# Performance work log

Measured on AMD Instinct MI355X. Metric: run time of the kernel, lower is better.

The kernel has to match this reference:

```python
import jax, jax.numpy as jnp
import numpy as np

N = 50000
E = 800000
IN_DIM = 256
HID = 256
OUT_DIM = 2


def setup_inputs() -> dict:
    key = jax.random.key(0)
    ks = jax.random.split(key, 10)
    x = jax.random.normal(ks[0], (N, IN_DIM), dtype=jnp.float32)
    edge_index = jax.random.randint(ks[1], (2, E), 0, N, dtype=jnp.int64)
    # Glorot-ish scaling so activations stay well-conditioned through 4 layers
    def w(k, fan_in, fan_out):
        return jax.random.normal(k, (fan_in, fan_out), dtype=jnp.float32) / jnp.sqrt(jnp.float32(fan_in))
    return {
        "x": x,
        "edge_index": edge_index,
        "W0": w(ks[2], IN_DIM, HID), "b0": jnp.zeros((HID,), jnp.float32),
        "W1": w(ks[3], HID, HID),    "b1": jnp.zeros((HID,), jnp.float32),
        "W2": w(ks[4], HID, HID),    "b2": jnp.zeros((HID,), jnp.float32),
        "W3": w(ks[5], HID, OUT_DIM), "b3": jnp.zeros((OUT_DIM,), jnp.float32),
    }


def _gcn_norm(edge_index, n, dtype):
    # PyG gcn_norm with self-loops: deg over destination, norm = d^-1/2[src]*d^-1/2[dst]
    loops = jnp.arange(n, dtype=edge_index.dtype)
    src = jnp.concatenate([edge_index[0], loops])
    dst = jnp.concatenate([edge_index[1], loops])
    deg = jax.ops.segment_sum(jnp.ones_like(dst, dtype=dtype), dst, num_segments=n)
    dis = deg ** -0.5  # deg >= 1 due to self-loops
    norm = dis[src] * dis[dst]
    return src, dst, norm


def reference(x, edge_index, W0, b0, W1, b1, W2, b2, W3, b3):
    n = x.shape[0]
    src, dst, norm = _gcn_norm(edge_index, n, x.dtype)

    def conv(h, W, b):
        h = h @ W                              # [N, F_out] dense GEMM
        msg = h[src] * norm[:, None]           # edge-gather + scale
        agg = jax.ops.segment_sum(msg, dst, num_segments=n)  # scatter-add
        return agg + b

    h = jax.nn.relu(conv(x, W0, b0))
    h = jax.nn.relu(conv(h, W1, b1))
    h = jax.nn.relu(conv(h, W2, b2))
    return conv(h, W3, b3)
```

## Files before the change

### kernel.cpp

```cpp
#include <hip/hip_runtime.h>

#define N_NODES 50000
#define N_EDGES 800000

static inline int cdiv(int a, int b) { return (a + b - 1) / b; }

typedef __attribute__((ext_vector_type(8))) short bf16x8;
typedef __attribute__((ext_vector_type(4))) float f32x4;
typedef __attribute__((ext_vector_type(2))) float f32x2;
typedef __attribute__((ext_vector_type(4))) unsigned int u32x4;

static __device__ __forceinline__ unsigned short f2bf(float f) {
    unsigned int u = __float_as_uint(f);
    unsigned int r = (u + 0x7FFF + ((u >> 16) & 1)) >> 16;
    return (unsigned short)r;
}
static __device__ __forceinline__ float bf2f(unsigned short h) {
    return __uint_as_float((unsigned int)h << 16);
}
static __device__ __forceinline__ float bf_lo(unsigned int u) { return __uint_as_float(u << 16); }
static __device__ __forceinline__ float bf_hi(unsigned int u) { return __uint_as_float(u & 0xFFFF0000u); }

static __device__ __forceinline__ int logc(int p) {
    int pl = p & 63;
    return (p & ~63) + (pl & 3) * 16 + (pl >> 2);
}

static __device__ __forceinline__ int2 ldnt2(const int2* p) {
    unsigned long long u = __builtin_nontemporal_load((const unsigned long long*)p);
    int2 r;
    r.x = (int)(u & 0xFFFFFFFFull);
    r.y = (int)(u >> 32);
    return r;
}

static __device__ __forceinline__ void acc8p(f32x2* acc, uint4 v, float wgt) {
    f32x2 w2;
    w2.x = wgt;
    w2.y = wgt;
    f32x2 p;
    p.x = bf_lo(v.x); p.y = bf_hi(v.x); acc[0] += p * w2;
    p.x = bf_lo(v.y); p.y = bf_hi(v.y); acc[1] += p * w2;
    p.x = bf_lo(v.z); p.y = bf_hi(v.z); acc[2] += p * w2;
    p.x = bf_lo(v.w); p.y = bf_hi(v.w); acc[3] += p * w2;
}


__global__ void k_count(const int* __restrict__ edst, int* cnt, int e) {
    int i = (blockIdx.x * 256 + threadIdx.x) * 4;
    if (i + 3 < e) {
        int4 v = *(const int4*)(edst + i);
        atomicAdd(&cnt[v.x], 1);
        atomicAdd(&cnt[v.y], 1);
        atomicAdd(&cnt[v.z], 1);
        atomicAdd(&cnt[v.w], 1);
    } else {
        for (int k = i; k < e; ++k) atomicAdd(&cnt[edst[k]], 1);
    }
}

__global__ __launch_bounds__(256) void k_scan1(const int* __restrict__ cnt,
                                               int* __restrict__ row_ptr,
                                               float* __restrict__ dis,
                                               int* __restrict__ blk, int n) {
    __shared__ int sums[256];
    int t = threadIdx.x;
    int base = blockIdx.x * 1024 + t * 4;
    int c0 = 0, c1 = 0, c2 = 0, c3 = 0;
    if (base + 3 < n) {
        int4 v = *(const int4*)(cnt + base);
        c0 = v.x + 1; c1 = v.y + 1; c2 = v.z + 1; c3 = v.w + 1;
    } else {
        if (base + 0 < n) c0 = cnt[base + 0] + 1;
        if (base + 1 < n) c1 = cnt[base + 1] + 1;
        if (base + 2 < n) c2 = cnt[base + 2] + 1;
        if (base + 3 < n) c3 = cnt[base + 3] + 1;
    }
    int s = c0 + c1 + c2 + c3;
    sums[t] = s;
    __syncthreads();
    int x = s;
    for (int off = 1; off < 256; off <<= 1) {
        int y = (t >= off) ? sums[t - off] : 0;
        __syncthreads();
        x += y;
        sums[t] = x;
        __syncthreads();
    }
    int excl = x - s;
    if (base + 0 < n) { row_ptr[base + 0] = excl;                dis[base + 0] = rsqrtf((float)c0); }
    if (base + 1 < n) { row_ptr[base + 1] = excl + c0;           dis[base + 1] = rsqrtf((float)c1); }
    if (base + 2 < n) { row_ptr[base + 2] = excl + c0 + c1;      dis[base + 2] = rsqrtf((float)c2); }
    if (base + 3 < n) { row_ptr[base + 3] = excl + c0 + c1 + c2; dis[base + 3] = rsqrtf((float)c3); }
    if (t == 255) blk[blockIdx.x] = x;
}

__global__ __launch_bounds__(256) void k_scan2(int* __restrict__ blk,
                                               int* __restrict__ row_ptr_n, int nb) {
    __shared__ int sums[256];
    int t = threadIdx.x;
    int s = (t < nb) ? blk[t] : 0;
    sums[t] = s;
    __syncthreads();
    int x = s;
    for (int off = 1; off < 256; off <<= 1) {
        int y = (t >= off) ? sums[t - off] : 0;
        __syncthreads();
        x += y;
        sums[t] = x;
        __syncthreads();
    }
    if (t < nb) blk[t] = x - s;
    if (t == 255) row_ptr_n[0] = x;
}

__global__ __launch_bounds__(256) void k_scan3(int* __restrict__ row_ptr,
                                               int* __restrict__ pos,
                                               const int* __restrict__ blk, int n) {
    int base = blockIdx.x * 1024 + threadIdx.x * 4;
    int off = blk[blockIdx.x];
#pragma unroll
    for (int i = 0; i < 4; ++i) {
        int idx = base + i;
        if (idx < n) {
            int v = row_ptr[idx] + off;
            row_ptr[idx] = v;
            pos[idx] = v;
        }
    }
}

__global__ void k_fill(const int* __restrict__ esrc, const int* __restrict__ edst,
                       int* pos, const float* __restrict__ dis,
                       int2* __restrict__ eg, int e, int n) {
    int i = blockIdx.x * 256 + threadIdx.x;
    if (i < e) {
        int s = esrc[i], d = edst[i];
        int p = atomicAdd(&pos[d], 1);
        unsigned long long u = (unsigned long long)(unsigned int)s |
                               ((unsigned long long)(unsigned int)__float_as_int(dis[s] * dis[d]) << 32);
        __builtin_nontemporal_store(u, (unsigned long long*)&eg[p]);
    } else if (i < e + n) {
        int v = i - e;
        int p = atomicAdd(&pos[v], 1);
        float dv = dis[v];
        unsigned long long u = (unsigned long long)(unsigned int)v |
                               ((unsigned long long)(unsigned int)__float_as_int(dv * dv) << 32);
        __builtin_nontemporal_store(u, (unsigned long long*)&eg[p]);
    }
}


__global__ __launch_bounds__(256) void k_prep(const float* __restrict__ W0,
                                              const float* __restrict__ W1,
                                              const float* __restrict__ W2,
                                              const float* __restrict__ b0,
                                              const float* __restrict__ b1,
                                              const float* __restrict__ b2,
                                              const float* __restrict__ W3,
                                              unsigned short* __restrict__ Wth,
                                              unsigned short* __restrict__ Wtl,
                                              float* __restrict__ bpw,
                                              const float* __restrict__ X,
                                              unsigned short* __restrict__ Xh, long total4) {
    if (blockIdx.x < 768) {
        int layer = blockIdx.x >> 8;
        int n = blockIdx.x & 255;
        int p = threadIdx.x;
        const float* W = layer == 0 ? W0 : (layer == 1 ? W1 : W2);
        int k = (layer != 0) ? logc(p) : p;
        float v = W[(size_t)k * 256 + n];
        unsigned short h = f2bf(v);
        size_t o = (size_t)layer * 65536 + (size_t)n * 256 + p;
        Wth[o] = h;
        Wtl[o] = f2bf(v - bf2f(h));
    } else if (blockIdx.x == 768) {
        int p = threadIdx.x;
        int c = logc(p);
        bpw[p] = b0[c];
        bpw[256 + p] = b1[c];
        bpw[512 + p] = b2[c];
        bpw[768 + p * 2 + 0] = W3[(size_t)c * 2 + 0];
        bpw[768 + p * 2 + 1] = W3[(size_t)c * 2 + 1];
    } else {
        long i = (long)(blockIdx.x - 769) * 256 + threadIdx.x;
        if (i >= total4) return;
        float4 v = *(const float4*)(X + i * 4);
        ushort4 h;
        h.x = f2bf(v.x);
        h.y = f2bf(v.y);
        h.z = f2bf(v.z);
        h.w = f2bf(v.w);
        *(ushort4*)(Xh + i * 4) = h;
    }
}


#define GEMM_RB 196

__global__ __launch_bounds__(256, 4) void k_gemm_mfma(const unsigned short* __restrict__ Ah,
                                                      const unsigned short* __restrict__ Wth,
                                                      const unsigned short* __restrict__ Wtl,
                                                      unsigned short* __restrict__ C, int M) {
    __shared__ unsigned short Wh[64][264];
    int rowblk = blockIdx.x % GEMM_RB;
    int colblk = blockIdx.x / GEMM_RB;
    int c0 = colblk * 64;
    int m0 = rowblk * 256;
    int t = threadIdx.x;
    int sr = t >> 2;

    {
        int hk0 = (t & 3) * 64;
        const unsigned short* gh = Wth + (size_t)(c0 + sr) * 256 + hk0;
        unsigned short* lh = &Wh[sr][hk0];
#pragma unroll
        for (int i = 0; i < 8; ++i)
            *(uint4*)(lh + i * 8) = *(const uint4*)(gh + i * 8);
    }
    __syncthreads();

    int lane = t & 63, wave = t >> 6;
    int quad = lane >> 4, l16 = lane & 15;

    const unsigned short* aph[4];
#pragma unroll
    for (int mt = 0; mt < 4; ++mt) {
        int m = m0 + wave * 64 + mt * 16 + l16;
        if (m >= M) m = M - 1;
        aph[mt] = Ah + (size_t)m * 256 + quad * 8;
    }
    const unsigned short* blp = Wtl + (size_t)(c0 + l16) * 256 + quad * 8;

    f32x4 acc[4][4];
#pragma unroll
    for (int i = 0; i < 4; ++i)
#pragma unroll
        for (int j = 0; j < 4; ++j) acc[i][j] = (f32x4){0.f, 0.f, 0.f, 0.f};

#pragma unroll 2
    for (int kc = 0; kc < 8; ++kc) {
        int ko = kc * 32;
        bf16x8 ahf[4];
#pragma unroll
        for (int mt = 0; mt < 4; ++mt) ahf[mt] = *(const bf16x8*)(aph[mt] + ko);
#pragma unroll
        for (int nt = 0; nt < 4; ++nt) {
            bf16x8 bh = *(const bf16x8*)&Wh[nt * 16 + l16][ko + quad * 8];
            bf16x8 bl = *(const bf16x8*)(blp + nt * 16 * 256 + ko);
#pragma unroll
            for (int mt = 0; mt < 4; ++mt) {
                acc[mt][nt] = __builtin_amdgcn_mfma_f32_16x16x32_bf16(ahf[mt], bh, acc[mt][nt], 0, 0, 0);
                acc[mt][nt] = __builtin_amdgcn_mfma_f32_16x16x32_bf16(ahf[mt], bl, acc[mt][nt], 0, 0, 0);
            }
        }
    }

#pragma unroll
    for (int mt = 0; mt < 4; ++mt) {
#pragma unroll
        for (int r = 0; r < 4; ++r) {
            int row = m0 + wave * 64 + mt * 16 + quad * 4 + r;
            if (row < M) {
                ushort4 sv;
                sv.x = f2bf(acc[mt][0][r]);
                sv.y = f2bf(acc[mt][1][r]);
                sv.z = f2bf(acc[mt][2][r]);
                sv.w = f2bf(acc[mt][3][r]);
                *(ushort4*)(C + (size_t)row * 256 + c0 + l16 * 4) = sv;
            }
        }
    }
}


template <int MODE>
__global__ __launch_bounds__(256, 8) void k_agg256(const unsigned short* __restrict__ t,
                                                   const int* __restrict__ row_ptr,
                                                   const int2* __restrict__ eg,
                                                   const float* __restrict__ bp,
                                                   unsigned short* __restrict__ outh,
                                                   const float* __restrict__ w3p,
                                                   float* __restrict__ t2, int n) {
    int lane = threadIdx.x & 63;
    int wave = threadIdx.x >> 6;
    int half = lane >> 5;
    int fl = lane & 31;
    const unsigned short* tp = t + fl * 8;
    int stride = gridDim.x * 4;

    for (int node = blockIdx.x * 4 + wave; node < n; node += stride) {
        int beg = row_ptr[node], end = row_ptr[node + 1];
        f32x2 acc2[4];
#pragma unroll
        for (int i = 0; i < 4; ++i) { acc2[i].x = 0.f; acc2[i].y = 0.f; }

        int e = beg + half;
        for (; e + 10 < end; e += 12) {
            int2 a0 = ldnt2(eg + e), a1 = ldnt2(eg + e + 2), a2 = ldnt2(eg + e + 4);
            int2 a3 = ldnt2(eg + e + 6), a4 = ldnt2(eg + e + 8), a5 = ldnt2(eg + e + 10);
            uint4 v0 = *(const uint4*)(tp + (size_t)a0.x * 256);
            uint4 v1 = *(const uint4*)(tp + (size_t)a1.x * 256);
            uint4 v2 = *(const uint4*)(tp + (size_t)a2.x * 256);
            uint4 v3 = *(const uint4*)(tp + (size_t)a3.x * 256);
            uint4 v4 = *(const uint4*)(tp + (size_t)a4.x * 256);
            uint4 v5 = *(const uint4*)(tp + (size_t)a5.x * 256);
            acc8p(acc2, v0, __int_as_float(a0.y));
            acc8p(acc2, v1, __int_as_float(a1.y));
            acc8p(acc2, v2, __int_as_float(a2.y));
            acc8p(acc2, v3, __int_as_float(a3.y));
            acc8p(acc2, v4, __int_as_float(a4.y));
            acc8p(acc2, v5, __int_as_float(a5.y));
        }
        for (; e + 6 < end; e += 8) {
            int2 a0 = ldnt2(eg + e), a1 = ldnt2(eg + e + 2);
            int2 a2 = ldnt2(eg + e + 4), a3 = ldnt2(eg + e + 6);
            uint4 v0 = *(const uint4*)(tp + (size_t)a0.x * 256);
            uint4 v1 = *(const uint4*)(tp + (size_t)a1.x * 256);
            uint4 v2 = *(const uint4*)(tp + (size_t)a2.x * 256);
            uint4 v3 = *(const uint4*)(tp + (size_t)a3.x * 256);
            acc8p(acc2, v0, __int_as_float(a0.y));
            acc8p(acc2, v1, __int_as_float(a1.y));
            acc8p(acc2, v2, __int_as_float(a2.y));
            acc8p(acc2, v3, __int_as_float(a3.y));
        }
        for (; e + 2 < end; e += 4) {
            int2 a0 = ldnt2(eg + e), a1 = ldnt2(eg + e + 2);
            uint4 v0 = *(const uint4*)(tp + (size_t)a0.x * 256);
            uint4 v1 = *(const uint4*)(tp + (size_t)a1.x * 256);
            acc8p(acc2, v0, __int_as_float(a0.y));
            acc8p(acc2, v1, __int_as_float(a1.y));
        }
        if (e < end) {
            int2 a0 = ldnt2(eg + e);
            uint4 v0 = *(const uint4*)(tp + (size_t)a0.x * 256);
            acc8p(acc2, v0, __int_as_float(a0.y));
        }

        float va[8];
#pragma unroll
        for (int i = 0; i < 4; ++i) { va[2 * i] = acc2[i].x; va[2 * i + 1] = acc2[i].y; }
#pragma unroll
        for (int i = 0; i < 8; ++i) va[i] += __shfl_xor(va[i], 32);

        if (MODE == 0) {
            if (half == 0) {
                float4 bA = *(const float4*)(bp + fl * 8);
                float4 bB = *(const float4*)(bp + fl * 8 + 4);
                float r0 = fmaxf(va[0] + bA.x, 0.f), r1 = fmaxf(va[1] + bA.y, 0.f);
                float r2 = fmaxf(va[2] + bA.z, 0.f), r3 = fmaxf(va[3] + bA.w, 0.f);
                float r4 = fmaxf(va[4] + bB.x, 0.f), r5 = fmaxf(va[5] + bB.y, 0.f);
                float r6 = fmaxf(va[6] + bB.z, 0.f), r7 = fmaxf(va[7] + bB.w, 0.f);
                u32x4 w;
                w.x = (unsigned)f2bf(r0) | ((unsigned)f2bf(r1) << 16);
                w.y = (unsigned)f2bf(r2) | ((unsigned)f2bf(r3) << 16);
                w.z = (unsigned)f2bf(r4) | ((unsigned)f2bf(r5) << 16);
                w.w = (unsigned)f2bf(r6) | ((unsigned)f2bf(r7) << 16);
                __builtin_nontemporal_store(w, (u32x4*)(outh + (size_t)node * 256 + fl * 8));
            }
        } else {
            float4 bA = *(const float4*)(bp + fl * 8);
            float4 bB = *(const float4*)(bp + fl * 8 + 4);
            float r0 = fmaxf(va[0] + bA.x, 0.f), r1 = fmaxf(va[1] + bA.y, 0.f);
            float r2 = fmaxf(va[2] + bA.z, 0.f), r3 = fmaxf(va[3] + bA.w, 0.f);
            float r4 = fmaxf(va[4] + bB.x, 0.f), r5 = fmaxf(va[5] + bB.y, 0.f);
            float r6 = fmaxf(va[6] + bB.z, 0.f), r7 = fmaxf(va[7] + bB.w, 0.f);
            const float* wp = w3p + fl * 16;
            float4 wA = *(const float4*)(wp + 0);
            float4 wB = *(const float4*)(wp + 4);
            float4 wC = *(const float4*)(wp + 8);
            float4 wD = *(const float4*)(wp + 12);
            float s0 = r0 * wA.x + r1 * wA.z + r2 * wB.x + r3 * wB.z +
                       r4 * wC.x + r5 * wC.z + r6 * wD.x + r7 * wD.z;
            float s1 = r0 * wA.y + r1 * wA.w + r2 * wB.y + r3 * wB.w +
                       r4 * wC.y + r5 * wC.w + r6 * wD.y + r7 * wD.w;
#pragma unroll
            for (int off = 16; off > 0; off >>= 1) {
                s0 += __shfl_xor(s0, off);
                s1 += __shfl_xor(s1, off);
            }
            if (lane == 0) {
                f32x2 o;
                o.x = s0;
                o.y = s1;
                __builtin_nontemporal_store(o, (f32x2*)(t2 + (size_t)node * 2));
            }
        }
    }
}


__global__ void k_agg2(const float* __restrict__ t2,
                       const int* __restrict__ row_ptr,
                       const int2* __restrict__ eg,
                       const float* __restrict__ b3,
                       float* __restrict__ out, int n) {
    int tid = blockIdx.x * 256 + threadIdx.x;
    int node = tid >> 2;
    int sub = tid & 3;
    if (node >= n) return;
    int beg = row_ptr[node], end = row_ptr[node + 1];
    float a0 = 0.f, a1 = 0.f;
    for (int e = beg + sub; e < end; e += 4) {
        int2 m = ldnt2(eg + e);
        float w = __int_as_float(m.y);
        float2 v = *(const float2*)(t2 + (size_t)m.x * 2);
        a0 += w * v.x;
        a1 += w * v.y;
    }
    a0 += __shfl_xor(a0, 1); a1 += __shfl_xor(a1, 1);
    a0 += __shfl_xor(a0, 2); a1 += __shfl_xor(a1, 2);
    if (sub == 0) {
        out[(size_t)node * 2 + 0] = a0 + b3[0];
        out[(size_t)node * 2 + 1] = a1 + b3[1];
    }
}


extern "C" void kernel_launch(void* const* d_in, const int* in_sizes, int n_in,
                              void* d_out, int out_size, void* d_ws, size_t ws_size,
                              hipStream_t stream) {
    const int N = N_NODES, E = N_EDGES;
    const float* x  = (const float*)d_in[0];
    const int* ei   = (const int*)d_in[1];
    const int* esrc = ei;
    const int* edst = ei + E;
    const float* W0 = (const float*)d_in[2];
    const float* b0 = (const float*)d_in[3];
    const float* W1 = (const float*)d_in[4];
    const float* b1 = (const float*)d_in[5];
    const float* W2 = (const float*)d_in[6];
    const float* b2 = (const float*)d_in[7];
    const float* W3 = (const float*)d_in[8];
    const float* b3 = (const float*)d_in[9];
    float* out = (float*)d_out;

    unsigned short* Ahh = (unsigned short*)d_ws;
    unsigned short* Tb  = Ahh + (size_t)N * 256;
    unsigned short* Wth = Tb + (size_t)N * 256;
    unsigned short* Wtl = Wth + 3 * 65536;
    int2*  eg     = (int2*)(Wtl + 3 * 65536);
    float* t2     = (float*)(eg + (E + N));
    float* bpw    = t2 + (size_t)N * 2;
    float* dis    = bpw + 1280;
    int*   cnt    = (int*)(dis + N);
    int*   row_ptr= cnt + N;
    int*   pos    = row_ptr + (N + 1);
    int*   blk    = pos + N;

    const int NB = cdiv(N, 1024);

    hipMemsetAsync(cnt, 0, (size_t)N * sizeof(int), stream);
    k_count<<<cdiv(E, 1024), 256, 0, stream>>>(edst, cnt, E);
    k_scan1<<<NB, 256, 0, stream>>>(cnt, row_ptr, dis, blk, N);
    k_scan2<<<1, 256, 0, stream>>>(blk, row_ptr + N, NB);
    k_scan3<<<NB, 256, 0, stream>>>(row_ptr, pos, blk, N);
    k_fill<<<cdiv(E + N, 256), 256, 0, stream>>>(esrc, edst, pos, dis, eg, E, N);

    const int ggrid = GEMM_RB * 4;
    const int agrid = 2048;
    const long total4 = (long)N * 64;
    const int CA = cdiv((int)total4, 256);

    k_prep<<<769 + CA, 256, 0, stream>>>(W0, W1, W2, b0, b1, b2, W3, Wth, Wtl, bpw, x, Ahh, total4);

    k_gemm_mfma<<<ggrid, 256, 0, stream>>>(Ahh, Wth, Wtl, Tb, N);
    k_agg256<0><<<agrid, 256, 0, stream>>>(Tb, row_ptr, eg, bpw, Ahh, nullptr, nullptr, N);
    k_gemm_mfma<<<ggrid, 256, 0, stream>>>(Ahh, Wth + 65536, Wtl + 65536, Tb, N);
    k_agg256<0><<<agrid, 256, 0, stream>>>(Tb, row_ptr, eg, bpw + 256, Ahh, nullptr, nullptr, N);
    k_gemm_mfma<<<ggrid, 256, 0, stream>>>(Ahh, Wth + 2 * 65536, Wtl + 2 * 65536, Tb, N);
    k_agg256<1><<<agrid, 256, 0, stream>>>(Tb, row_ptr, eg, bpw + 512, nullptr, bpw + 768, t2, N);
    k_agg2<<<cdiv(4 * N, 256), 256, 0, stream>>>(t2, row_ptr, eg, b3, out, N);
}
```

Baseline: 568.8 us.

## Store GEMM output in 32-column slices and aggregate per slice for cache locality

The GEMM now writes its output as eight 32-column slices, each a contiguous N x 32 array, instead of row-major 256-wide rows. The aggregation kernel assigns each block to one slice, so the gathered working set per slice is about 3.2 MB and can stay in L2/LLC while the random neighbour gathers run. Each lane now reads only 4 bytes per edge, with 4 edge groups per wave, and the final layer reduces partial W3 products across slices using float atomics into a zeroed t2. In exchange, gathers become much finer-grained, the edge lists are read eight times, and the atomics make the float summation order nondeterministic.

```diff
diff --git a/kernel.cpp b/kernel.cpp
--- a/kernel.cpp
+++ b/kernel.cpp
@@ -8,7 +8,6 @@
 typedef __attribute__((ext_vector_type(8))) short bf16x8;
 typedef __attribute__((ext_vector_type(4))) float f32x4;
 typedef __attribute__((ext_vector_type(2))) float f32x2;
-typedef __attribute__((ext_vector_type(4))) unsigned int u32x4;
 
 static __device__ __forceinline__ unsigned short f2bf(float f) {
     unsigned int u = __float_as_uint(f);
@@ -32,17 +31,6 @@
     r.x = (int)(u & 0xFFFFFFFFull);
     r.y = (int)(u >> 32);
     return r;
-}
-
-static __device__ __forceinline__ void acc8p(f32x2* acc, uint4 v, float wgt) {
-    f32x2 w2;
-    w2.x = wgt;
-    w2.y = wgt;
-    f32x2 p;
-    p.x = bf_lo(v.x); p.y = bf_hi(v.x); acc[0] += p * w2;
-    p.x = bf_lo(v.y); p.y = bf_hi(v.y); acc[1] += p * w2;
-    p.x = bf_lo(v.z); p.y = bf_hi(v.z); acc[2] += p * w2;
-    p.x = bf_lo(v.w); p.y = bf_hi(v.w); acc[3] += p * w2;
 }
 
 
@@ -197,6 +185,7 @@
 
 
 #define GEMM_RB 196
+#define SLICE_STRIDE ((size_t)N_NODES * 32)
 
 __global__ __launch_bounds__(256, 4) void k_gemm_mfma(const unsigned short* __restrict__ Ah,
                                                       const unsigned short* __restrict__ Wth,
@@ -256,6 +245,9 @@
         }
     }
 
+    int slice = colblk * 2 + (l16 >> 3);
+    int icol = (l16 & 7) * 4;
+    unsigned short* cs = C + (size_t)slice * SLICE_STRIDE + icol;
 #pragma unroll
     for (int mt = 0; mt < 4; ++mt) {
 #pragma unroll
@@ -267,7 +259,7 @@
                 sv.y = f2bf(acc[mt][1][r]);
                 sv.z = f2bf(acc[mt][2][r]);
                 sv.w = f2bf(acc[mt][3][r]);
-                *(ushort4*)(C + (size_t)row * 256 + c0 + l16 * 4) = sv;
+                *(ushort4*)(cs + (size_t)row * 32) = sv;
             }
         }
     }
@@ -275,115 +267,70 @@
 
 
 template <int MODE>
-__global__ __launch_bounds__(256, 8) void k_agg256(const unsigned short* __restrict__ t,
-                                                   const int* __restrict__ row_ptr,
-                                                   const int2* __restrict__ eg,
-                                                   const float* __restrict__ bp,
-                                                   unsigned short* __restrict__ outh,
-                                                   const float* __restrict__ w3p,
-                                                   float* __restrict__ t2, int n) {
+__global__ __launch_bounds__(256, 8) void k_aggs(const unsigned short* __restrict__ t,
+                                                 const int* __restrict__ row_ptr,
+                                                 const int2* __restrict__ eg,
+                                                 const float* __restrict__ bp,
+                                                 unsigned short* __restrict__ outh,
+                                                 const float* __restrict__ w3p,
+                                                 float* __restrict__ t2, int n) {
     int lane = threadIdx.x & 63;
     int wave = threadIdx.x >> 6;
-    int half = lane >> 5;
-    int fl = lane & 31;
-    const unsigned short* tp = t + fl * 8;
-    int stride = gridDim.x * 4;
-
-    for (int node = blockIdx.x * 4 + wave; node < n; node += stride) {
+    int g = lane >> 4, li = lane & 15;
+    int slice = blockIdx.x & 7;
+    int chunk = blockIdx.x >> 3;
+    const unsigned short* ts = t + (size_t)slice * SLICE_STRIDE + li * 2;
+    int p = slice * 32 + li * 2;
+
+    float2 bb = *(const float2*)(bp + p);
+    float w00 = 0.f, w01 = 0.f, w10 = 0.f, w11 = 0.f;
+    if (MODE == 1) {
+        float4 ww = *(const float4*)(w3p + p * 2);
+        w00 = ww.x; w01 = ww.y; w10 = ww.z; w11 = ww.w;
+    }
+
+    for (int node = chunk * 4 + wave; node < n; node += 1024) {
         int beg = row_ptr[node], end = row_ptr[node + 1];
-        f32x2 acc2[4];
-#pragma unroll
-        for (int i = 0; i < 4; ++i) { acc2[i].x = 0.f; acc2[i].y = 0.f; }
-
-        int e = beg + half;
-        for (; e + 10 < end; e += 12) {
-            int2 a0 = ldnt2(eg + e), a1 = ldnt2(eg + e + 2), a2 = ldnt2(eg + e + 4);
-            int2 a3 = ldnt2(eg + e + 6), a4 = ldnt2(eg + e + 8), a5 = ldnt2(eg + e + 10);
-            uint4 v0 = *(const uint4*)(tp + (size_t)a0.x * 256);
-            uint4 v1 = *(const uint4*)(tp + (size_t)a1.x * 256);
-            uint4 v2 = *(const uint4*)(tp + (size_t)a2.x * 256);
-            uint4 v3 = *(const uint4*)(tp + (size_t)a3.x * 256);
-            uint4 v4 = *(const uint4*)(tp + (size_t)a4.x * 256);
-            uint4 v5 = *(const uint4*)(tp + (size_t)a5.x * 256);
-            acc8p(acc2, v0, __int_as_float(a0.y));
-            acc8p(acc2, v1, __int_as_float(a1.y));
-            acc8p(acc2, v2, __int_as_float(a2.y));
-            acc8p(acc2, v3, __int_as_float(a3.y));
-            acc8p(acc2, v4, __int_as_float(a4.y));
-            acc8p(acc2, v5, __int_as_float(a5.y));
+        float a0 = 0.f, a1 = 0.f;
+        int e = beg + g;
+        if (e < end) {
+            int2 rec = ldnt2(eg + e);
+            for (e += 4; e < end; e += 4) {
+                int2 nx = ldnt2(eg + e);
+                unsigned v = *(const unsigned*)(ts + (size_t)rec.x * 32);
+                float w = __int_as_float(rec.y);
+                a0 += w * bf_lo(v);
+                a1 += w * bf_hi(v);
+                rec = nx;
+            }
+            unsigned v = *(const unsigned*)(ts + (size_t)rec.x * 32);
+            float w = __int_as_float(rec.y);
+            a0 += w * bf_lo(v);
+            a1 += w * bf_hi(v);
         }
-        for (; e + 6 < end; e += 8) {
-            int2 a0 = ldnt2(eg + e), a1 = ldnt2(eg + e + 2);
-            int2 a2 = ldnt2(eg + e + 4), a3 = ldnt2(eg + e + 6);
-            uint4 v0 = *(const uint4*)(tp + (size_t)a0.x * 256);
-            uint4 v1 = *(const uint4*)(tp + (size_t)a1.x * 256);
-            uint4 v2 = *(const uint4*)(tp + (size_t)a2.x * 256);
-            uint4 v3 = *(const uint4*)(tp + (size_t)a3.x * 256);
-            acc8p(acc2, v0, __int_as_float(a0.y));
-            acc8p(acc2, v1, __int_as_float(a1.y));
-            acc8p(acc2, v2, __int_as_float(a2.y));
-            acc8p(acc2, v3, __int_as_float(a3.y));
-        }
-        for (; e + 2 < end; e += 4) {
-            int2 a0 = ldnt2(eg + e), a1 = ldnt2(eg + e + 2);
-            uint4 v0 = *(const uint4*)(tp + (size_t)a0.x * 256);
-            uint4 v1 = *(const uint4*)(tp + (size_t)a1.x * 256);
-            acc8p(acc2, v0, __int_as_float(a0.y));
-            acc8p(acc2, v1, __int_as_float(a1.y));
-        }
-        if (e < end) {
-            int2 a0 = ldnt2(eg + e);
-            uint4 v0 = *(const uint4*)(tp + (size_t)a0.x * 256);
-            acc8p(acc2, v0, __int_as_float(a0.y));
-        }
-
-        float va[8];
-#pragma unroll
-        for (int i = 0; i < 4; ++i) { va[2 * i] = acc2[i].x; va[2 * i + 1] = acc2[i].y; }
-#pragma unroll
-        for (int i = 0; i < 8; ++i) va[i] += __shfl_xor(va[i], 32);
+        a0 += __shfl_xor(a0, 16); a1 += __shfl_xor(a1, 16);
+        a0 += __shfl_xor(a0, 32); a1 += __shfl_xor(a1, 32);
 
         if (MODE == 0) {
-            if (half == 0) {
-                float4 bA = *(const float4*)(bp + fl * 8);
-                float4 bB = *(const float4*)(bp + fl * 8 + 4);
-                float r0 = fmaxf(va[0] + bA.x, 0.f), r1 = fmaxf(va[1] + bA.y, 0.f);
-                float r2 = fmaxf(va[2] + bA.z, 0.f), r3 = fmaxf(va[3] + bA.w, 0.f);
-                float r4 = fmaxf(va[4] + bB.x, 0.f), r5 = fmaxf(va[5] + bB.y, 0.f);
-                float r6 = fmaxf(va[6] + bB.z, 0.f), r7 = fmaxf(va[7] + bB.w, 0.f);
-                u32x4 w;
-                w.x = (unsigned)f2bf(r0) | ((unsigned)f2bf(r1) << 16);
-                w.y = (unsigned)f2bf(r2) | ((unsigned)f2bf(r3) << 16);
-                w.z = (unsigned)f2bf(r4) | ((unsigned)f2bf(r5) << 16);
-                w.w = (unsigned)f2bf(r6) | ((unsigned)f2bf(r7) << 16);
-                __builtin_nontemporal_store(w, (u32x4*)(outh + (size_t)node * 256 + fl * 8));
+            if (g == 0) {
+                float r0 = fmaxf(a0 + bb.x, 0.f), r1 = fmaxf(a1 + bb.y, 0.f);
+                unsigned pk = (unsigned)f2bf(r0) | ((unsigned)f2bf(r1) << 16);
+                __builtin_nontemporal_store(pk, (unsigned*)(outh + (size_t)node * 256 + p));
             }
         } else {
-            float4 bA = *(const float4*)(bp + fl * 8);
-            float4 bB = *(const float4*)(bp + fl * 8 + 4);
-            float r0 = fmaxf(va[0] + bA.x, 0.f), r1 = fmaxf(va[1] + bA.y, 0.f);
-            float r2 = fmaxf(va[2] + bA.z, 0.f), r3 = fmaxf(va[3] + bA.w, 0.f);
-            float r4 = fmaxf(va[4] + bB.x, 0.f), r5 = fmaxf(va[5] + bB.y, 0.f);
-            float r6 = fmaxf(va[6] + bB.z, 0.f), r7 = fmaxf(va[7] + bB.w, 0.f);
-            const float* wp = w3p + fl * 16;
-            float4 wA = *(const float4*)(wp + 0);
-            float4 wB = *(const float4*)(wp + 4);
-            float4 wC = *(const float4*)(wp + 8);
-            float4 wD = *(const float4*)(wp + 12);
-            float s0 = r0 * wA.x + r1 * wA.z + r2 * wB.x + r3 * wB.z +
-                       r4 * wC.x + r5 * wC.z + r6 * wD.x + r7 * wD.z;
-            float s1 = r0 * wA.y + r1 * wA.w + r2 * wB.y + r3 * wB.w +
-                       r4 * wC.y + r5 * wC.w + r6 * wD.y + r7 * wD.w;
-#pragma unroll
-            for (int off = 16; off > 0; off >>= 1) {
-                s0 += __shfl_xor(s0, off);
-                s1 += __shfl_xor(s1, off);
-            }
+            float s0 = 0.f, s1 = 0.f;
+            if (g == 0) {
+                float r0 = fmaxf(a0 + bb.x, 0.f), r1 = fmaxf(a1 + bb.y, 0.f);
+                s0 = r0 * w00 + r1 * w10;
+                s1 = r0 * w01 + r1 * w11;
+            }
+            s0 += __shfl_xor(s0, 1); s1 += __shfl_xor(s1, 1);
+            s0 += __shfl_xor(s0, 2); s1 += __shfl_xor(s1, 2);
+            s0 += __shfl_xor(s0, 4); s1 += __shfl_xor(s1, 4);
+            s0 += __shfl_xor(s0, 8); s1 += __shfl_xor(s1, 8);
             if (lane == 0) {
-                f32x2 o;
-                o.x = s0;
-                o.y = s1;
-                __builtin_nontemporal_store(o, (f32x2*)(t2 + (size_t)node * 2));
+                atomicAdd(&t2[(size_t)node * 2 + 0], s0);
+                atomicAdd(&t2[(size_t)node * 2 + 1], s1);
             }
         }
     }
@@ -451,6 +398,7 @@
     const int NB = cdiv(N, 1024);
 
     hipMemsetAsync(cnt, 0, (size_t)N * sizeof(int), stream);
+    hipMemsetAsync(t2, 0, (size_t)N * 2 * sizeof(float), stream);
     k_count<<<cdiv(E, 1024), 256, 0, stream>>>(edst, cnt, E);
     k_scan1<<<NB, 256, 0, stream>>>(cnt, row_ptr, dis, blk, N);
     k_scan2<<<1, 256, 0, stream>>>(blk, row_ptr + N, NB);
@@ -465,10 +413,10 @@
     k_prep<<<769 + CA, 256, 0, stream>>>(W0, W1, W2, b0, b1, b2, W3, Wth, Wtl, bpw, x, Ahh, total4);
 
     k_gemm_mfma<<<ggrid, 256, 0, stream>>>(Ahh, Wth, Wtl, Tb, N);
-    k_agg256<0><<<agrid, 256, 0, stream>>>(Tb, row_ptr, eg, bpw, Ahh, nullptr, nullptr, N);
+    k_aggs<0><<<agrid, 256, 0, stream>>>(Tb, row_ptr, eg, bpw, Ahh, nullptr, nullptr, N);
     k_gemm_mfma<<<ggrid, 256, 0, stream>>>(Ahh, Wth + 65536, Wtl + 65536, Tb, N);
-    k_agg256<0><<<agrid, 256, 0, stream>>>(Tb, row_ptr, eg, bpw + 256, Ahh, nullptr, nullptr, N);
+    k_aggs<0><<<agrid, 256, 0, stream>>>(Tb, row_ptr, eg, bpw + 256, Ahh, nullptr, nullptr, N);
     k_gemm_mfma<<<ggrid, 256, 0, stream>>>(Ahh, Wth + 2 * 65536, Wtl + 2 * 65536, Tb, N);
-    k_agg256<1><<<agrid, 256, 0, stream>>>(Tb, row_ptr, eg, bpw + 512, nullptr, bpw + 768, t2, N);
+    k_aggs<1><<<agrid, 256, 0, stream>>>(Tb, row_ptr, eg, bpw + 512, nullptr, bpw + 768, t2, N);
     k_agg2<<<cdiv(4 * N, 256), 256, 0, stream>>>(t2, row_ptr, eg, b3, out, N);
 }
```

Result: slower. 972.0 us (+70.9%).
